# Kernel tuning notes

Hardware: AMD Instinct MI355X
Metric: run time of the kernel (lower is better)

The kernel has to match this reference:

```python
import jax, jax.numpy as jnp
import numpy as np

NEG_SLOPE = 0.2  # PyG GATConv default


def gat_conv(x, edge_index, W, att_src, att_dst, bias, heads, out_c, concat):
    """One PyG-style GATConv layer (eval mode, add_self_loops=True)."""
    N = x.shape[0]
    loop = jnp.arange(N, dtype=edge_index.dtype)
    src = jnp.concatenate([edge_index[0], loop])  # [E+N]
    dst = jnp.concatenate([edge_index[1], loop])
    h = (x @ W).reshape(N, heads, out_c)                     # [N,H,C]
    a_src = jnp.einsum('nhc,hc->nh', h, att_src)             # [N,H]
    a_dst = jnp.einsum('nhc,hc->nh', h, att_dst)
    e = jax.nn.leaky_relu(a_src[src] + a_dst[dst], NEG_SLOPE)  # [E+N,H]
    # segment softmax over incoming edges of each dst node (self-loops guarantee non-empty segments)
    emax = jax.ops.segment_max(e, dst, num_segments=N)
    e = jnp.exp(e - emax[dst])
    denom = jax.ops.segment_sum(e, dst, num_segments=N)
    alpha = e / denom[dst]                                   # [E+N,H]
    msg = h[src] * alpha[:, :, None]                         # [E+N,H,C]
    out = jax.ops.segment_sum(msg, dst, num_segments=N)      # [N,H,C]
    out = out.reshape(N, heads * out_c) if concat else out.mean(axis=1)
    return out + bias


def setup_inputs() -> dict:
    key = jax.random.key(0)
    ks = jax.random.split(key, 10)
    N, E, Fin, Hc, H, Out = 20000, 320000, 256, 128, 4, 256
    s = lambda k, shp: jax.random.normal(k, shp, dtype=jnp.float32) * 0.05
    return {
        'x': jax.random.normal(ks[0], (N, Fin), dtype=jnp.float32),
        'edge_index': jax.random.randint(ks[1], (2, E), 0, N, dtype=jnp.int64),
        'W1': s(ks[2], (Fin, H * Hc)),
        'att_src1': s(ks[3], (H, Hc)),
        'att_dst1': s(ks[4], (H, Hc)),
        'b1': s(ks[5], (H * Hc,)),
        'W2': s(ks[6], (H * Hc, Out)),
        'att_src2': s(ks[7], (1, Out)),
        'att_dst2': s(ks[8], (1, Out)),
        'b2': s(ks[9], (Out,)),
    }


def reference(x, edge_index, W1, att_src1, att_dst1, b1, W2, att_src2, att_dst2, b2):
    h = gat_conv(x, edge_index, W1, att_src1, att_dst1, b1, heads=4, out_c=128, concat=True)
    h = jax.nn.gelu(h, approximate=False)  # torch.nn.GELU default is exact
    out = gat_conv(h, edge_index, W2, att_src2, att_dst2, b2, heads=1, out_c=256, concat=False)
    return out
```

## Files before the change

kernel.cpp:

```cpp
#include <hip/hip_runtime.h>
#include <hip/hip_bf16.h>

#define NODES 20000
#define EDGES 320000
#define FIN   256
#define HEADS 4
#define C1    128
#define F1    512
#define F2    256
#define TOT_E (EDGES + NODES)
#define MAXDEG 64

typedef __bf16 bf16x8 __attribute__((ext_vector_type(8)));
typedef float  f32x4  __attribute__((ext_vector_type(4)));
typedef unsigned short ushort_t;
typedef ushort_t ushx8 __attribute__((ext_vector_type(8)));

#define GLOAD_LDS16(gp, lp) \
    __builtin_amdgcn_global_load_lds((const __attribute__((address_space(1))) void*)(gp), \
                                     (__attribute__((address_space(3))) void*)(lp), 16, 0, 0)

__device__ __forceinline__ float bf2f(ushort_t u) {
    union { unsigned int i; float f; } c; c.i = ((unsigned)u) << 16; return c.f;
}
__device__ __forceinline__ ushort_t f2bf(float f) {
    union { float f; unsigned int i; } c; c.f = f;
    unsigned r = (c.i + 0x7fffu + ((c.i >> 16) & 1u)) >> 16;
    return (ushort_t)r;
}
__device__ __forceinline__ float lrelu(float v) { return (v > 0.f) ? v : 0.2f * v; }

#define CAST_T (NODES * FIN / 4)
#define T1N    (FIN * F1)
#define T2N    (F1 * F2)
#define PREP_T (CAST_T + T1N + T2N + 512 + TOT_E)
__global__ void k_prep(const float* __restrict__ x, ushort_t* __restrict__ x_bf,
                       const float* __restrict__ W1, ushort_t* __restrict__ w1t,
                       const float* __restrict__ W2, ushort_t* __restrict__ w2t,
                       const float* __restrict__ attS2, const float* __restrict__ attD2,
                       float* __restrict__ w2s, float* __restrict__ w2d,
                       const int* __restrict__ ei, int* __restrict__ counts,
                       int* __restrict__ csr) {
    int t = blockIdx.x * 256 + threadIdx.x;
    if (t < CAST_T) {
        int i = t * 4;
        float4 v = *reinterpret_cast<const float4*>(x + i);
        ushort4 o;
        o.x = f2bf(v.x); o.y = f2bf(v.y); o.z = f2bf(v.z); o.w = f2bf(v.w);
        *reinterpret_cast<ushort4*>(x_bf + i) = o;
    } else if (t < CAST_T + T1N) {
        int idx = t - CAST_T;
        int n = idx >> 8, k = idx & 255;
        w1t[idx] = f2bf(W1[k * F1 + n]);
    } else if (t < CAST_T + T1N + T2N) {
        int idx = t - CAST_T - T1N;
        int n = idx >> 9, k = idx & 511;
        w2t[idx] = f2bf(W2[k * F2 + n]);
    } else if (t < CAST_T + T1N + T2N + 512) {
        int f = t - CAST_T - T1N - T2N;
        const float* row = W2 + (size_t)f * F2;
        float s = 0.f, d = 0.f;
        for (int o = 0; o < F2; o++) { float v = row[o]; s += v * attS2[o]; d += v * attD2[o]; }
        w2s[f] = s; w2d[f] = d;
    } else if (t < PREP_T) {
        int e = t - CAST_T - T1N - T2N - 512;
        int src, dst;
        if (e < EDGES) { src = ei[e]; dst = ei[EDGES + e]; }
        else           { src = dst = e - EDGES; }
        int pos = atomicAdd(&counts[dst], 1);
        csr[dst * MAXDEG + pos] = src;
    }
}

__launch_bounds__(256)
__global__ void k_gemm_att(const ushort_t* __restrict__ A, const ushort_t* __restrict__ Bt,
                           ushort_t* __restrict__ Cbf, int M, int N, int K,
                           const float* __restrict__ attS, const float* __restrict__ attD,
                           float* __restrict__ aS, float* __restrict__ aD, int aStride,
                           int doAtt) {
    __shared__ ushort_t lA[128 * 64];
    __shared__ ushort_t lB[128 * 64];
    const int tid  = threadIdx.x;
    const int lane = tid & 63, w = tid >> 6;
    const int wr = w >> 1, wc = w & 1;
    const int row0 = blockIdx.x * 128;
    const int col0 = blockIdx.y * 128;
    f32x4 acc[4][4] = {};

    const int srow = lane >> 3;
    const int scol = ((lane & 7) ^ srow) * 8;

    for (int k0 = 0; k0 < K; k0 += 64) {
        #pragma unroll
        for (int p = 0; p < 4; p++) {
            int rb = p * 32 + w * 8;
            GLOAD_LDS16(&A[(size_t)(row0 + rb + srow) * K + k0 + scol], &lA[rb * 64]);
            GLOAD_LDS16(&Bt[(size_t)(col0 + rb + srow) * K + k0 + scol], &lB[rb * 64]);
        }
        __syncthreads();
        #pragma unroll
        for (int kk = 0; kk < 2; kk++) {
            const int q = lane >> 4;
            const int sw = ((kk * 4 + q) ^ (lane & 7)) * 8;
            bf16x8 af[4], bfr[4];
            #pragma unroll
            for (int m = 0; m < 4; m++)
                af[m] = *reinterpret_cast<const bf16x8*>(&lA[(wr * 64 + m * 16 + (lane & 15)) * 64 + sw]);
            #pragma unroll
            for (int n = 0; n < 4; n++)
                bfr[n] = *reinterpret_cast<const bf16x8*>(&lB[(wc * 64 + n * 16 + (lane & 15)) * 64 + sw]);
            #pragma unroll
            for (int m = 0; m < 4; m++)
                #pragma unroll
                for (int n = 0; n < 4; n++)
                    acc[m][n] = __builtin_amdgcn_mfma_f32_16x16x32_bf16(af[m], bfr[n], acc[m][n], 0, 0, 0);
        }
        __syncthreads();
    }

    #pragma unroll
    for (int m = 0; m < 4; m++) {
        int gr0 = row0 + wr * 64 + m * 16 + (lane >> 4) * 4;
        #pragma unroll
        for (int n = 0; n < 4; n++) {
            int gc = col0 + wc * 64 + n * 16 + (lane & 15);
            #pragma unroll
            for (int r = 0; r < 4; r++) {
                int gr = gr0 + r;
                if (gr < M) Cbf[(size_t)gr * N + gc] = f2bf(acc[m][n][r]);
            }
        }
    }

    if (!doAtt) return;
    float pds[16], pdd[16];
    #pragma unroll
    for (int i = 0; i < 16; i++) { pds[i] = 0.f; pdd[i] = 0.f; }
    const int attBase = blockIdx.y * 128;
    #pragma unroll
    for (int n = 0; n < 4; n++) {
        int colr = wc * 64 + n * 16 + (lane & 15);
        float av = attS[attBase + colr];
        float dv = attD[attBase + colr];
        #pragma unroll
        for (int m = 0; m < 4; m++)
            #pragma unroll
            for (int r = 0; r < 4; r++) {
                pds[m * 4 + r] += acc[m][n][r] * av;
                pdd[m * 4 + r] += acc[m][n][r] * dv;
            }
    }
    #pragma unroll
    for (int o = 1; o < 16; o <<= 1) {
        #pragma unroll
        for (int i = 0; i < 16; i++) {
            pds[i] += __shfl_xor(pds[i], o);
            pdd[i] += __shfl_xor(pdd[i], o);
        }
    }
    if ((lane & 15) == 0) {
        int hoff = blockIdx.y;
        #pragma unroll
        for (int m = 0; m < 4; m++)
            #pragma unroll
            for (int r = 0; r < 4; r++) {
                int gr = row0 + wr * 64 + m * 16 + (lane >> 4) * 4 + r;
                if (gr < M) {
                    atomicAdd(&aS[gr * aStride + hoff], pds[m * 4 + r]);
                    atomicAdd(&aD[gr * aStride + hoff], pdd[m * 4 + r]);
                }
            }
    }
}

__launch_bounds__(256)
__global__ void k_agg1(const ushort_t* __restrict__ h1, const int* __restrict__ counts,
                       const int* __restrict__ csr,
                       const float* __restrict__ a_src, const float* __restrict__ a_dst,
                       const float* __restrict__ b1, ushort_t* __restrict__ hgelu) {
    int w = threadIdx.x >> 6, lane = threadIdx.x & 63;
    int d = blockIdx.x * 4 + w;
    int h = lane >> 4;
    int off = d * MAXDEG, deg = counts[d];
    float adst = a_dst[d * HEADS + h];
    float acc[8] = {};
    float den = 0.f;
    int j = 0;
    for (; j + 4 <= deg; j += 4) {
        int s0 = csr[off + j + 0];
        int s1 = csr[off + j + 1];
        int s2 = csr[off + j + 2];
        int s3 = csr[off + j + 3];
        ushx8 v0 = *reinterpret_cast<const ushx8*>(&h1[(size_t)s0 * F1 + lane * 8]);
        ushx8 v1 = *reinterpret_cast<const ushx8*>(&h1[(size_t)s1 * F1 + lane * 8]);
        ushx8 v2 = *reinterpret_cast<const ushx8*>(&h1[(size_t)s2 * F1 + lane * 8]);
        ushx8 v3 = *reinterpret_cast<const ushx8*>(&h1[(size_t)s3 * F1 + lane * 8]);
        float w0 = __expf(lrelu(a_src[s0 * HEADS + h] + adst));
        float w1 = __expf(lrelu(a_src[s1 * HEADS + h] + adst));
        float w2 = __expf(lrelu(a_src[s2 * HEADS + h] + adst));
        float w3 = __expf(lrelu(a_src[s3 * HEADS + h] + adst));
        den += (w0 + w1) + (w2 + w3);
        #pragma unroll
        for (int i = 0; i < 8; i++)
            acc[i] += w0 * bf2f(v0[i]) + w1 * bf2f(v1[i]) + w2 * bf2f(v2[i]) + w3 * bf2f(v3[i]);
    }
    for (; j < deg; j++) {
        int s = csr[off + j];
        ushx8 hv = *reinterpret_cast<const ushx8*>(&h1[(size_t)s * F1 + lane * 8]);
        float wgt = __expf(lrelu(a_src[s * HEADS + h] + adst));
        den += wgt;
        #pragma unroll
        for (int i = 0; i < 8; i++) acc[i] += wgt * bf2f(hv[i]);
    }
    float inv = 1.f / den;
    int c0 = lane * 8;
    ushx8 o;
    #pragma unroll
    for (int i = 0; i < 8; i++) {
        float v = acc[i] * inv + b1[c0 + i];
        v = 0.5f * v * (1.f + erff(v * 0.70710678118654752f));
        o[i] = f2bf(v);
    }
    *reinterpret_cast<ushx8*>(&hgelu[(size_t)d * F1 + c0]) = o;
}

__launch_bounds__(256)
__global__ void k_att2(const ushort_t* __restrict__ hg, const float* __restrict__ w2s,
                       const float* __restrict__ w2d, float* __restrict__ as2,
                       float* __restrict__ ad2) {
    int w = threadIdx.x >> 6, lane = threadIdx.x & 63;
    int n = blockIdx.x * 4 + w;
    ushx8 v = *reinterpret_cast<const ushx8*>(&hg[(size_t)n * F1 + lane * 8]);
    int c0 = lane * 8;
    float s = 0.f, d = 0.f;
    #pragma unroll
    for (int i = 0; i < 8; i++) {
        float f = bf2f(v[i]);
        s += f * w2s[c0 + i];
        d += f * w2d[c0 + i];
    }
    #pragma unroll
    for (int o = 1; o < 64; o <<= 1) { s += __shfl_xor(s, o); d += __shfl_xor(d, o); }
    if (lane == 0) { as2[n] = s; ad2[n] = d; }
}

__launch_bounds__(256)
__global__ void k_agg2(const ushort_t* __restrict__ h2, const int* __restrict__ counts,
                       const int* __restrict__ csr,
                       const float* __restrict__ a_src, const float* __restrict__ a_dst,
                       const float* __restrict__ b2, float* __restrict__ out) {
    int w = threadIdx.x >> 6, lane = threadIdx.x & 63;
    int d = blockIdx.x * 4 + w;
    int off = d * MAXDEG, deg = counts[d];
    int half = lane >> 5, il = lane & 31;
    float adst = a_dst[d];
    float acc[8] = {};
    float den = 0.f;
    int j = 0;
    for (; j + 8 <= deg; j += 8) {
        int s0 = csr[off + j + 0 + half];
        int s1 = csr[off + j + 2 + half];
        int s2 = csr[off + j + 4 + half];
        int s3 = csr[off + j + 6 + half];
        ushx8 v0 = *reinterpret_cast<const ushx8*>(&h2[(size_t)s0 * F2 + il * 8]);
        ushx8 v1 = *reinterpret_cast<const ushx8*>(&h2[(size_t)s1 * F2 + il * 8]);
        ushx8 v2 = *reinterpret_cast<const ushx8*>(&h2[(size_t)s2 * F2 + il * 8]);
        ushx8 v3 = *reinterpret_cast<const ushx8*>(&h2[(size_t)s3 * F2 + il * 8]);
        float w0 = __expf(lrelu(a_src[s0] + adst));
        float w1 = __expf(lrelu(a_src[s1] + adst));
        float w2 = __expf(lrelu(a_src[s2] + adst));
        float w3 = __expf(lrelu(a_src[s3] + adst));
        den += (w0 + w1) + (w2 + w3);
        #pragma unroll
        for (int i = 0; i < 8; i++)
            acc[i] += w0 * bf2f(v0[i]) + w1 * bf2f(v1[i]) + w2 * bf2f(v2[i]) + w3 * bf2f(v3[i]);
    }
    for (; j < deg; j += 2) {
        int jj = j + half;
        if (jj < deg) {
            int s = csr[off + jj];
            ushx8 hv = *reinterpret_cast<const ushx8*>(&h2[(size_t)s * F2 + il * 8]);
            float wgt = __expf(lrelu(a_src[s] + adst));
            den += wgt;
            #pragma unroll
            for (int i = 0; i < 8; i++) acc[i] += wgt * bf2f(hv[i]);
        }
    }
    den += __shfl_xor(den, 32);
    #pragma unroll
    for (int i = 0; i < 8; i++) acc[i] += __shfl_xor(acc[i], 32);
    if (half == 0) {
        float inv = 1.f / den;
        int c0 = il * 8;
        float4 o0, o1;
        o0.x = acc[0] * inv + b2[c0 + 0];
        o0.y = acc[1] * inv + b2[c0 + 1];
        o0.z = acc[2] * inv + b2[c0 + 2];
        o0.w = acc[3] * inv + b2[c0 + 3];
        o1.x = acc[4] * inv + b2[c0 + 4];
        o1.y = acc[5] * inv + b2[c0 + 5];
        o1.z = acc[6] * inv + b2[c0 + 6];
        o1.w = acc[7] * inv + b2[c0 + 7];
        *reinterpret_cast<float4*>(&out[(size_t)d * F2 + c0])     = o0;
        *reinterpret_cast<float4*>(&out[(size_t)d * F2 + c0 + 4]) = o1;
    }
}

extern "C" void kernel_launch(void* const* d_in, const int* in_sizes, int n_in,
                              void* d_out, int out_size, void* d_ws, size_t ws_size,
                              hipStream_t stream) {
    const float* x        = (const float*)d_in[0];
    const int*   ei       = (const int*)d_in[1];
    const float* W1       = (const float*)d_in[2];
    const float* att_src1 = (const float*)d_in[3];
    const float* att_dst1 = (const float*)d_in[4];
    const float* b1       = (const float*)d_in[5];
    const float* W2       = (const float*)d_in[6];
    const float* att_src2 = (const float*)d_in[7];
    const float* att_dst2 = (const float*)d_in[8];
    const float* b2       = (const float*)d_in[9];
    float* out = (float*)d_out;

    char* p = (char*)d_ws;
    auto alloc = [&](size_t bytes) -> char* {
        char* r = p; p += (bytes + 255) & ~(size_t)255; return r;
    };
    ushort_t* x_bf  = (ushort_t*)alloc((size_t)NODES * FIN * 2);
    ushort_t* w1t   = (ushort_t*)alloc((size_t)F1 * FIN * 2);
    ushort_t* w2t   = (ushort_t*)alloc((size_t)F2 * F1 * 2);
    ushort_t* h1    = (ushort_t*)alloc((size_t)NODES * F1 * 2);
    ushort_t* hg    = (ushort_t*)alloc((size_t)NODES * F1 * 2);
    ushort_t* h2    = x_bf;
    char* zbase     = p;
    int* counts     = (int*)alloc((size_t)NODES * 4);
    float* as1      = (float*)alloc((size_t)NODES * HEADS * 4);
    float* ad1      = (float*)alloc((size_t)NODES * HEADS * 4);
    size_t zspan    = (size_t)(p - zbase);
    float* as2      = (float*)alloc((size_t)NODES * 4);
    float* ad2      = (float*)alloc((size_t)NODES * 4);
    float* w2s      = (float*)alloc((size_t)F1 * 4);
    float* w2d      = (float*)alloc((size_t)F1 * 4);
    int* csr        = (int*)alloc((size_t)NODES * MAXDEG * 4);

    hipMemsetAsync(zbase, 0, zspan, stream);
    k_prep<<<(PREP_T + 255) / 256, 256, 0, stream>>>(x, x_bf, W1, w1t, W2, w2t,
                                                     att_src2, att_dst2, w2s, w2d,
                                                     ei, counts, csr);
    k_gemm_att<<<dim3(157, 4), 256, 0, stream>>>(x_bf, w1t, h1, NODES, F1, FIN,
                                                 att_src1, att_dst1, as1, ad1, HEADS, 1);
    k_agg1<<<NODES / 4, 256, 0, stream>>>(h1, counts, csr, as1, ad1, b1, hg);
    k_att2<<<NODES / 4, 256, 0, stream>>>(hg, w2s, w2d, as2, ad2);
    k_gemm_att<<<dim3(157, 2), 256, 0, stream>>>(hg, w2t, h2, NODES, F2, F1,
                                                 nullptr, nullptr, nullptr, nullptr, 1, 0);
    k_agg2<<<NODES / 4, 256, 0, stream>>>(h2, counts, csr, as2, ad2, b2, out);
}
```

Before: 241.5 us.

## Double-buffer GEMM LDS tiles and replace attention-score atomics with LDS reduction

The bf16 MFMA GEMM now uses two LDS buffers, so the global-to-LDS loads for the next K tile are issued before the current tile's MFMAs run, overlapping memory and compute. The attention-logit epilogue no longer does global float atomicAdds from both column-waves. One wave pair writes its partial sums to LDS and the other adds them and stores the result directly. Because the stores overwrite, the memset of the as1/ad1 buffers is dropped and only the degree counters are still zeroed. The cost is doubled LDS per block (about 65 KB), which limits how many blocks fit per CU, plus an extra block barrier in the epilogue.

```diff
diff --git a/kernel.cpp b/kernel.cpp
--- a/kernel.cpp
+++ b/kernel.cpp
@@ -78,8 +78,9 @@
                            const float* __restrict__ attS, const float* __restrict__ attD,
                            float* __restrict__ aS, float* __restrict__ aD, int aStride,
                            int doAtt) {
-    __shared__ ushort_t lA[128 * 64];
-    __shared__ ushort_t lB[128 * 64];
+    __shared__ ushort_t lA[2][128 * 64];
+    __shared__ ushort_t lB[2][128 * 64];
+    __shared__ float redS[128], redD[128];
     const int tid  = threadIdx.x;
     const int lane = tid & 63, w = tid >> 6;
     const int wr = w >> 1, wc = w & 1;
@@ -90,14 +91,21 @@
     const int srow = lane >> 3;
     const int scol = ((lane & 7) ^ srow) * 8;
 
-    for (int k0 = 0; k0 < K; k0 += 64) {
+    auto stage = [&](int buf, int k0) {
         #pragma unroll
         for (int p = 0; p < 4; p++) {
             int rb = p * 32 + w * 8;
-            GLOAD_LDS16(&A[(size_t)(row0 + rb + srow) * K + k0 + scol], &lA[rb * 64]);
-            GLOAD_LDS16(&Bt[(size_t)(col0 + rb + srow) * K + k0 + scol], &lB[rb * 64]);
-        }
-        __syncthreads();
+            GLOAD_LDS16(&A[(size_t)(row0 + rb + srow) * K + k0 + scol], &lA[buf][rb * 64]);
+            GLOAD_LDS16(&Bt[(size_t)(col0 + rb + srow) * K + k0 + scol], &lB[buf][rb * 64]);
+        }
+    };
+
+    const int NT = K >> 6;
+    stage(0, 0);
+    __syncthreads();
+    for (int t = 0; t < NT; t++) {
+        const int cur = t & 1;
+        if (t + 1 < NT) stage(cur ^ 1, (t + 1) << 6);
         #pragma unroll
         for (int kk = 0; kk < 2; kk++) {
             const int q = lane >> 4;
@@ -105,10 +113,10 @@
             bf16x8 af[4], bfr[4];
             #pragma unroll
             for (int m = 0; m < 4; m++)
-                af[m] = *reinterpret_cast<const bf16x8*>(&lA[(wr * 64 + m * 16 + (lane & 15)) * 64 + sw]);
+                af[m] = *reinterpret_cast<const bf16x8*>(&lA[cur][(wr * 64 + m * 16 + (lane & 15)) * 64 + sw]);
             #pragma unroll
             for (int n = 0; n < 4; n++)
-                bfr[n] = *reinterpret_cast<const bf16x8*>(&lB[(wc * 64 + n * 16 + (lane & 15)) * 64 + sw]);
+                bfr[n] = *reinterpret_cast<const bf16x8*>(&lB[cur][(wc * 64 + n * 16 + (lane & 15)) * 64 + sw]);
             #pragma unroll
             for (int m = 0; m < 4; m++)
                 #pragma unroll
@@ -158,16 +166,28 @@
             pdd[i] += __shfl_xor(pdd[i], o);
         }
     }
-    if ((lane & 15) == 0) {
+    if (wc == 0 && (lane & 15) == 0) {
+        #pragma unroll
+        for (int m = 0; m < 4; m++)
+            #pragma unroll
+            for (int r = 0; r < 4; r++) {
+                int rowloc = wr * 64 + m * 16 + (lane >> 4) * 4 + r;
+                redS[rowloc] = pds[m * 4 + r];
+                redD[rowloc] = pdd[m * 4 + r];
+            }
+    }
+    __syncthreads();
+    if (wc == 1 && (lane & 15) == 0) {
         int hoff = blockIdx.y;
         #pragma unroll
         for (int m = 0; m < 4; m++)
             #pragma unroll
             for (int r = 0; r < 4; r++) {
-                int gr = row0 + wr * 64 + m * 16 + (lane >> 4) * 4 + r;
+                int rowloc = wr * 64 + m * 16 + (lane >> 4) * 4 + r;
+                int gr = row0 + rowloc;
                 if (gr < M) {
-                    atomicAdd(&aS[gr * aStride + hoff], pds[m * 4 + r]);
-                    atomicAdd(&aD[gr * aStride + hoff], pdd[m * 4 + r]);
+                    aS[gr * aStride + hoff] = pds[m * 4 + r] + redS[rowloc];
+                    aD[gr * aStride + hoff] = pdd[m * 4 + r] + redD[rowloc];
                 }
             }
     }
@@ -331,18 +351,16 @@
     ushort_t* h1    = (ushort_t*)alloc((size_t)NODES * F1 * 2);
     ushort_t* hg    = (ushort_t*)alloc((size_t)NODES * F1 * 2);
     ushort_t* h2    = x_bf;
-    char* zbase     = p;
     int* counts     = (int*)alloc((size_t)NODES * 4);
     float* as1      = (float*)alloc((size_t)NODES * HEADS * 4);
     float* ad1      = (float*)alloc((size_t)NODES * HEADS * 4);
-    size_t zspan    = (size_t)(p - zbase);
     float* as2      = (float*)alloc((size_t)NODES * 4);
     float* ad2      = (float*)alloc((size_t)NODES * 4);
     float* w2s      = (float*)alloc((size_t)F1 * 4);
     float* w2d      = (float*)alloc((size_t)F1 * 4);
     int* csr        = (int*)alloc((size_t)NODES * MAXDEG * 4);
 
-    hipMemsetAsync(zbase, 0, zspan, stream);
+    hipMemsetAsync(counts, 0, (size_t)NODES * 4, stream);
     k_prep<<<(PREP_T + 255) / 256, 256, 0, stream>>>(x, x_bf, W1, w1t, W2, w2t,
                                                      att_src2, att_dst2, w2s, w2d,
                                                      ei, counts, csr);
```

New measurement: 234.0 us. 1.03x faster.
